# Optimization experiments

Hardware: AMD Instinct MI355X
Metric: run time of the kernel (lower is better)

Reference implementation:

```python
import jax, jax.numpy as jnp
import numpy as np

B, S, D, H = 2, 4096, 512, 8
DK = D // H


def setup_inputs() -> dict:
    key = jax.random.key(0)
    ks = jax.random.split(key, 8)
    q = jax.random.normal(ks[0], (B, S, D), dtype=jnp.float32)
    k = jax.random.normal(ks[1], (B, S, D), dtype=jnp.float32)
    v = jax.random.normal(ks[2], (B, S, D), dtype=jnp.float32)
    mask = jax.random.randint(ks[3], (B, S, S), 0, 2, dtype=jnp.int32)
    scale = 1.0 / np.sqrt(D)
    w_q = jax.random.normal(ks[4], (D, D), dtype=jnp.float32) * scale
    w_k = jax.random.normal(ks[5], (D, D), dtype=jnp.float32) * scale
    w_v = jax.random.normal(ks[6], (D, D), dtype=jnp.float32) * scale
    w_o = jax.random.normal(ks[7], (D, D), dtype=jnp.float32) * scale
    return {"q": q, "k": k, "v": v, "mask": mask,
            "w_q": w_q, "w_k": w_k, "w_v": w_v, "w_o": w_o}


def reference(q, k, v, mask, w_q, w_k, w_v, w_o):
    # Projections (weights stored as [in, out]; no bias, matching bias=False)
    # [B,S,D] -> [B,H,S,DK]
    def split_heads(x):
        return x.reshape(B, S, H, DK).transpose(0, 2, 1, 3)

    qh = split_heads(q @ w_q)
    kh = split_heads(k @ w_k)
    vh = split_heads(v @ w_v)

    inv_sqrt_dk = jnp.float32(1.0 / np.sqrt(DK))
    # Explicit O(S^2) score matrix, as in the original module
    scores = jnp.einsum('bhqd,bhkd->bhqk', qh, kh) * inv_sqrt_dk
    scores = jnp.where(mask[:, None, :, :] == 0, jnp.float32(-1e9), scores)
    attn = jax.nn.softmax(scores, axis=-1)
    # dropout in eval mode (p=0) -> identity
    x = jnp.einsum('bhqk,bhkd->bhqd', attn, vh)
    x = x.transpose(0, 2, 1, 3).reshape(B, S, D)
    return x @ w_o
```

## Files before the change

kernel.cpp:

```cpp
#include <hip/hip_runtime.h>
#include <hip/hip_bf16.h>

#define Bn 2
#define Sn 4096
#define Dn 512
#define Hn 8
#define DKn 64

typedef __attribute__((ext_vector_type(8))) short bf16x8;
typedef __attribute__((ext_vector_type(4))) float f32x4;
typedef __attribute__((ext_vector_type(4))) _Float16 f16x4;
typedef __attribute__((ext_vector_type(8))) _Float16 f16x8;
typedef __attribute__((ext_vector_type(2))) _Float16 f16x2;
typedef __attribute__((ext_vector_type(8))) unsigned short us8;
typedef __attribute__((ext_vector_type(4))) unsigned short us4;

__device__ __forceinline__ unsigned short f2bf(float f) {
  unsigned u = __builtin_bit_cast(unsigned, f);
  u += 0x7fffu + ((u >> 16) & 1u);
  return (unsigned short)(u >> 16);
}

__device__ __forceinline__ unsigned cvtpk_bf16(float lo, float hi) {
  unsigned r;
  asm("v_cvt_pk_bf16_f32 %0, %1, %2" : "=v"(r) : "v"(lo), "v"(hi));
  return r;
}

__device__ __forceinline__ unsigned spread4(unsigned x) {
  x = (x | (x << 12)) & 0x000F000Fu;
  x = (x | (x << 6)) & 0x03030303u;
  x = (x | (x << 3)) & 0x11111111u;
  return x;
}

__global__ __launch_bounds__(256) void prep_k(
    const int* __restrict__ mask, unsigned int* __restrict__ pm,
    const float* __restrict__ wq, const float* __restrict__ wk,
    const float* __restrict__ wv, const float* __restrict__ wo,
    unsigned short* __restrict__ wt) {
  const int t = threadIdx.x;
  if (blockIdx.x < 256) {
    __shared__ unsigned short ls[64][68];
    int bid = blockIdx.x;
    int z = bid >> 6, x = bid & 7, y = (bid >> 3) & 7;
    const float* W = z == 0 ? wq : z == 1 ? wk : z == 2 ? wv : wo;
    const float wsc = (z == 0) ? 0.18033688011112042f : 1.0f;
    int k0 = x * 64, n0 = y * 64;
    for (int j = 0; j < 4; ++j) {
      int i = t + j * 256;
      int r = i >> 4, c4 = (i & 15) << 2;
      float4 f = *(const float4*)&W[(size_t)(k0 + r) * 512 + n0 + c4];
      ls[c4 + 0][r] = f2bf(f.x * wsc);
      ls[c4 + 1][r] = f2bf(f.y * wsc);
      ls[c4 + 2][r] = f2bf(f.z * wsc);
      ls[c4 + 3][r] = f2bf(f.w * wsc);
    }
    __syncthreads();
    unsigned short* out = wt + (size_t)z * 512 * 512;
    for (int j = 0; j < 4; ++j) {
      int i = t + j * 256;
      int r = i >> 4, c4 = (i & 15) << 2;
      us4 v = {ls[r][c4], ls[r][c4 + 1], ls[r][c4 + 2], ls[r][c4 + 3]};
      *(us4*)&out[(size_t)(n0 + r) * 512 + k0 + c4] = v;
    }
  } else {
    size_t gt = (size_t)(blockIdx.x - 256) * 256 + t;
    for (int it = 0; it < 8; ++it, gt += 1048576) {
      size_t e0 = gt * 4;
      int4 mv = *(const int4*)&mask[e0];
      unsigned long long bl0 = __ballot(mv.x != 0);
      unsigned long long bl1 = __ballot(mv.y != 0);
      unsigned long long bl2 = __ballot(mv.z != 0);
      unsigned long long bl3 = __ballot(mv.w != 0);
      if ((t & 63) < 8) {
        int wd = t & 7;
        unsigned word = spread4((unsigned)(bl0 >> (wd * 8)) & 0xFFu) |
                        (spread4((unsigned)(bl1 >> (wd * 8)) & 0xFFu) << 1) |
                        (spread4((unsigned)(bl2 >> (wd * 8)) & 0xFFu) << 2) |
                        (spread4((unsigned)(bl3 >> (wd * 8)) & 0xFFu) << 3);
        size_t eb = e0 & ~(size_t)255;
        int qq = (int)((eb >> 12) & 4095);
        int bb = (int)(eb >> 24);
        int kvw = (int)((eb >> 5) & 127) + wd;
        pm[((size_t)bb * 128 + kvw) * 4096 + qq] = word;
      }
    }
  }
}

template <int MT, bool HEADS>
__global__ __launch_bounds__(256, 2) void gemm_k(
    const float* __restrict__ aq, const float* __restrict__ ak,
    const float* __restrict__ av, const unsigned short* __restrict__ abf,
    const unsigned short* __restrict__ wt, unsigned short* __restrict__ oh,
    unsigned short* __restrict__ vtg, float* __restrict__ olin) {
  __shared__ unsigned short smem[MT * 8192 + 16384];
  const int z = blockIdx.z;
  const float* A32 = HEADS ? (z == 0 ? aq : z == 1 ? ak : av) : nullptr;
  const unsigned short* Wt = wt + (size_t)z * 512 * 512;
  const int m0 = blockIdx.x * (MT * 64), n0 = blockIdx.y * 128;
  const int t = threadIdx.x, w = t >> 6, l = t & 63;
  const int quad = l >> 4, c = l & 15;

  f32x4 acc[MT][8] = {};
  us8 apre[MT * 2], bpre[4];

  auto ldA = [&](int j, int kk) -> us8 {
    int i = t + j * 256, r = i >> 3, u = i & 7;
    if constexpr (HEADS) {
      const float* s = &A32[(size_t)(m0 + r) * 512 + kk + (u << 3)];
      float4 f0 = *(const float4*)s;
      float4 f1 = *(const float4*)(s + 4);
      uint4 p;
      p.x = cvtpk_bf16(f0.x, f0.y);
      p.y = cvtpk_bf16(f0.z, f0.w);
      p.z = cvtpk_bf16(f1.x, f1.y);
      p.w = cvtpk_bf16(f1.z, f1.w);
      return __builtin_bit_cast(us8, p);
    } else {
      return *(const us8*)&abf[(size_t)(m0 + r) * 512 + kk + (u << 3)];
    }
  };

#pragma unroll
  for (int j = 0; j < MT * 2; ++j) apre[j] = ldA(j, 0);
#pragma unroll
  for (int j = 0; j < 4; ++j) {
    int i = t + j * 256, r = i >> 3, u = i & 7;
    bpre[j] = *(const us8*)&Wt[(size_t)(n0 + r) * 512 + (u << 3)];
  }
#pragma unroll
  for (int j = 0; j < MT * 2; ++j) {
    int i = t + j * 256, r = i >> 3, u = i & 7;
    *(us8*)&smem[r * 64 + ((u ^ (r & 7)) << 3)] = apre[j];
  }
#pragma unroll
  for (int j = 0; j < 4; ++j) {
    int i = t + j * 256, r = i >> 3, u = i & 7;
    *(us8*)&smem[MT * 8192 + r * 64 + ((u ^ (r & 7)) << 3)] = bpre[j];
  }

  for (int k0 = 0; k0 < 512; k0 += 64) {
    const int cur = (k0 >> 6) & 1;
    const unsigned short* AsC = &smem[cur * (MT * 4096)];
    const unsigned short* BsC = &smem[MT * 8192 + cur * 8192];
    __syncthreads();
    const bool nxt = k0 + 64 < 512;
    if (nxt) {
#pragma unroll
      for (int j = 0; j < MT * 2; ++j) apre[j] = ldA(j, k0 + 64);
#pragma unroll
      for (int j = 0; j < 4; ++j) {
        int i = t + j * 256, r = i >> 3, u = i & 7;
        bpre[j] = *(const us8*)&Wt[(size_t)(n0 + r) * 512 + k0 + 64 + (u << 3)];
      }
    }

#pragma unroll
    for (int kc = 0; kc < 2; ++kc) {
      bf16x8 aA[MT], bB[8];
      int u = kc * 4 + quad;
#pragma unroll
      for (int mt = 0; mt < MT; ++mt) {
        int row = w * (MT * 16) + mt * 16 + c;
        aA[mt] = *(const bf16x8*)&AsC[row * 64 + ((u ^ (c & 7)) << 3)];
      }
#pragma unroll
      for (int nt = 0; nt < 8; ++nt) {
        int row = nt * 16 + c;
        bB[nt] = *(const bf16x8*)&BsC[row * 64 + ((u ^ (c & 7)) << 3)];
      }
      __builtin_amdgcn_s_setprio(1);
#pragma unroll
      for (int mt = 0; mt < MT; ++mt)
#pragma unroll
        for (int nt = 0; nt < 8; ++nt)
          acc[mt][nt] = __builtin_amdgcn_mfma_f32_16x16x32_bf16(
              aA[mt], bB[nt], acc[mt][nt], 0, 0, 0);
      __builtin_amdgcn_s_setprio(0);
    }

    if (nxt) {
      unsigned short* AsN = &smem[(cur ^ 1) * (MT * 4096)];
      unsigned short* BsN = &smem[MT * 8192 + (cur ^ 1) * 8192];
#pragma unroll
      for (int j = 0; j < MT * 2; ++j) {
        int i = t + j * 256, r = i >> 3, u = i & 7;
        *(us8*)&AsN[r * 64 + ((u ^ (r & 7)) << 3)] = apre[j];
      }
#pragma unroll
      for (int j = 0; j < 4; ++j) {
        int i = t + j * 256, r = i >> 3, u = i & 7;
        *(us8*)&BsN[r * 64 + ((u ^ (r & 7)) << 3)] = bpre[j];
      }
    }
  }

  if constexpr (HEADS) {
    if (z == 2) {
      __syncthreads();
#pragma unroll
      for (int mt = 0; mt < MT; ++mt) {
        int mb = w * (MT * 16) + mt * 16 + (quad << 2);
        int ml = (mb & 64) | (((mb >> 5) & 1) << 5) | (((mb >> 2) & 3) << 3) |
                 (((mb >> 4) & 1) << 2);
#pragma unroll
        for (int nt = 0; nt < 8; ++nt) {
          int nl = nt * 16 + c;
          us4 pk;
#pragma unroll
          for (int r = 0; r < 4; ++r)
            pk[r] = __builtin_bit_cast(unsigned short, (_Float16)acc[mt][nt][r]);
          *(us4*)&smem[nl * 152 + ml] = pk;
        }
      }
      __syncthreads();
      const int bb = m0 >> 12, sb = m0 & 4095;
#pragma unroll
      for (int j = 0; j < MT * 4; ++j) {
        int i = t + j * 256;
        int nl = i >> 4, mc = (i & 15) << 3;
        us8 vv = *(const us8*)&smem[nl * 152 + mc];
        int n = n0 + nl, hh = n >> 6, dk = n & 63;
        *(us8*)&vtg[((size_t)(bb * Hn + hh) * DKn + dk) * Sn + sb + mc] = vv;
      }
    } else {
#pragma unroll
      for (int mt = 0; mt < MT; ++mt)
#pragma unroll
        for (int nt = 0; nt < 8; ++nt) {
          int m = m0 + w * (MT * 16) + mt * 16 + (quad << 2);
          int n = n0 + nt * 16 + c;
          int b = m >> 12, s = m & 4095, hh = n >> 6, dk = n & 63;
          unsigned short* dst = &oh[(size_t)z * (Bn * Hn * Sn * DKn) +
                                    ((size_t)(b * Hn + hh) * Sn + s) * DKn + dk];
          unsigned pk0 = cvtpk_bf16(acc[mt][nt][0], acc[mt][nt][1]);
          unsigned pk1 = cvtpk_bf16(acc[mt][nt][2], acc[mt][nt][3]);
          dst[0] = (unsigned short)pk0;
          dst[DKn] = (unsigned short)(pk0 >> 16);
          dst[2 * DKn] = (unsigned short)pk1;
          dst[3 * DKn] = (unsigned short)(pk1 >> 16);
        }
    }
  } else {
#pragma unroll
    for (int mt = 0; mt < MT; ++mt)
#pragma unroll
      for (int nt = 0; nt < 8; ++nt)
#pragma unroll
        for (int r = 0; r < 4; ++r) {
          int m = m0 + w * (MT * 16) + mt * 16 + (quad << 2) + r;
          int n = n0 + nt * 16 + c;
          olin[(size_t)m * 512 + n] = acc[mt][nt][r];
        }
  }
}

__global__ __launch_bounds__(512, 4) void flash_k(
    const unsigned short* __restrict__ Qh, const unsigned short* __restrict__ Kh,
    const unsigned short* __restrict__ VtG, const unsigned int* __restrict__ pmt,
    unsigned short* __restrict__ attn) {
  __shared__ unsigned short Ks[2][2][64 * 64];
  __shared__ unsigned short Vts[2][2][64 * 64];
  __shared__ unsigned int Mw[2][2][256];
  __shared__ unsigned long long MskT[16];

  const int bid = blockIdx.x;
  const int h = bid & 7;
  const int b = (bid >> 3) & 1;
  const int q0 = (bid >> 4) * 128;
  const int t = threadIdx.x;
  const int g = t >> 8, tg = t & 255;
  const int w = (t >> 6) & 3, l = t & 63;
  const int quad = l >> 4, c = l & 15;
  const size_t hb = (size_t)(b * Hn + h) * Sn * DKn;
  const unsigned short* Qg = Qh + hb;

  if (t < 16) {
    unsigned lo = ((t & 1) ? 0xFFFFu : 0u) | ((t & 2) ? 0xFFFF0000u : 0u);
    unsigned hi = ((t & 4) ? 0xFFFFu : 0u) | ((t & 8) ? 0xFFFF0000u : 0u);
    MskT[t] = ((unsigned long long)hi << 32) | lo;
  }

  bf16x8 bQ[2][2];
#pragma unroll
  for (int qf = 0; qf < 2; ++qf) {
    int qrow = q0 + w * 32 + qf * 16 + c;
#pragma unroll
    for (int kc = 0; kc < 2; ++kc)
      bQ[qf][kc] = *(const bf16x8*)&Qg[(size_t)qrow * 64 + kc * 32 + quad * 8];
  }

  f32x4 oacc[2][4] = {};
  f32x4 oaccl[2] = {};
  f16x8 vone8;
#pragma unroll
  for (int i = 0; i < 8; ++i) vone8[i] = (_Float16)1.0f;

  const int sr = tg >> 3, su = tg & 7;
  const int off0 = sr * 64 + ((su ^ (sr & 7)) << 3);
  const int off1 = (sr + 32) * 64 + ((su ^ (sr & 7)) << 3);

  const unsigned short* kp0 = Kh + hb + ((size_t)(g * 64 + sr)) * 64 + (su << 3);
  const unsigned short* kp1 = kp0 + 32 * 64;
  const unsigned short* vp0 = VtG + hb + (size_t)sr * Sn + g * 64 + (su << 3);
  const unsigned short* vp1 = VtG + hb + (size_t)(sr + 32) * Sn + g * 64 + (su << 3);
  const unsigned int* mp =
      pmt + ((size_t)b * 128 + g * 2 + (tg >> 7)) * 4096 + q0 + (tg & 127);

  us8 kpre[2], vpre[2];
  unsigned mpre;
  kpre[0] = *(const us8*)kp0;
  kpre[1] = *(const us8*)kp1;
  vpre[0] = *(const us8*)vp0;
  vpre[1] = *(const us8*)vp1;
  mpre = *mp;
  *(us8*)&Ks[g][0][off0] = kpre[0];
  *(us8*)&Ks[g][0][off1] = kpre[1];
  *(us8*)&Vts[g][0][off0] = vpre[0];
  *(us8*)&Vts[g][0][off1] = vpre[1];
  Mw[g][0][tg] = mpre;

  for (int it = 0; it < 32; ++it) {
    const int cur = it & 1;
    __syncthreads();
    const bool nxt = it + 1 < 32;
    if (nxt) {
      kp0 += 8192; kp1 += 8192; vp0 += 128; vp1 += 128; mp += 16384;
      kpre[0] = *(const us8*)kp0;
      kpre[1] = *(const us8*)kp1;
      vpre[0] = *(const us8*)vp0;
      vpre[1] = *(const us8*)vp1;
      mpre = *mp;
    }

    f32x4 sacc[2][4] = {};
#pragma unroll
    for (int kc = 0; kc < 2; ++kc) {
      int u = kc * 4 + quad;
#pragma unroll
      for (int kvt = 0; kvt < 4; ++kvt) {
        int row = kvt * 16 + c;
        bf16x8 aK = *(const bf16x8*)&Ks[g][cur][row * 64 + ((u ^ (c & 7)) << 3)];
#pragma unroll
        for (int qf = 0; qf < 2; ++qf)
          sacc[qf][kvt] = __builtin_amdgcn_mfma_f32_16x16x32_bf16(
              aK, bQ[qf][kc], sacc[qf][kvt], 0, 0, 0);
      }
    }

    f16x8 ph[2][2];
#pragma unroll
    for (int qf = 0; qf < 2; ++qf) {
      int qloc = w * 32 + qf * 16 + c;
      unsigned mv0 = Mw[g][cur][qloc] >> (quad << 2);
      unsigned mv1 = Mw[g][cur][128 + qloc] >> (quad << 2);
#pragma unroll
      for (int half = 0; half < 2; ++half) {
        unsigned wd = half ? mv1 : mv0;
        uint4 ww;
#pragma unroll
        for (int kvh = 0; kvh < 2; ++kvh) {
          const f32x4 s4 = sacc[qf][half * 2 + kvh];
          unsigned long long mk = MskT[(wd >> (kvh << 4)) & 15u];
          unsigned a = __builtin_bit_cast(
              unsigned, __builtin_amdgcn_cvt_pkrtz(
                            __builtin_amdgcn_exp2f(s4[0]),
                            __builtin_amdgcn_exp2f(s4[1])));
          unsigned bpk = __builtin_bit_cast(
              unsigned, __builtin_amdgcn_cvt_pkrtz(
                            __builtin_amdgcn_exp2f(s4[2]),
                            __builtin_amdgcn_exp2f(s4[3])));
          (&ww.x)[kvh * 2] = a & (unsigned)mk;
          (&ww.x)[kvh * 2 + 1] = bpk & (unsigned)(mk >> 32);
        }
        ph[qf][half] = __builtin_bit_cast(f16x8, ww);
      }
    }

#pragma unroll
    for (int half = 0; half < 2; ++half) {
      int u2 = half * 4 + quad;
#pragma unroll
      for (int dkt = 0; dkt < 4; ++dkt) {
        int dk = dkt * 16 + c;
        f16x8 bV = __builtin_bit_cast(
            f16x8, *(const us8*)&Vts[g][cur][dk * 64 + ((u2 ^ (c & 7)) << 3)]);
#pragma unroll
        for (int qf = 0; qf < 2; ++qf)
          oacc[qf][dkt] = __builtin_amdgcn_mfma_f32_16x16x32_f16(
              ph[qf][half], bV, oacc[qf][dkt], 0, 0, 0);
      }
#pragma unroll
      for (int qf = 0; qf < 2; ++qf)
        oaccl[qf] = __builtin_amdgcn_mfma_f32_16x16x32_f16(
            ph[qf][half], vone8, oaccl[qf], 0, 0, 0);
    }

    if (nxt) {
      const int nb = cur ^ 1;
      *(us8*)&Ks[g][nb][off0] = kpre[0];
      *(us8*)&Ks[g][nb][off1] = kpre[1];
      *(us8*)&Vts[g][nb][off0] = vpre[0];
      *(us8*)&Vts[g][nb][off1] = vpre[1];
      Mw[g][nb][tg] = mpre;
    }
  }

  __syncthreads();
  float* fsum = (float*)&Ks[0][0][0];
  float* flsum = (float*)&Vts[0][0][0];
  if (g == 1) {
#pragma unroll
    for (int qf = 0; qf < 2; ++qf) {
#pragma unroll
      for (int dkt = 0; dkt < 4; ++dkt)
        *(f32x4*)&fsum[(((qf * 4 + dkt) * 4 + w) * 64 + l) * 4] = oacc[qf][dkt];
      *(f32x4*)&flsum[((qf * 4 + w) * 64 + l) * 4] = oaccl[qf];
    }
  }
  __syncthreads();
  if (g == 0) {
#pragma unroll
    for (int qf = 0; qf < 2; ++qf) {
      f32x4 l1 = *(const f32x4*)&flsum[((qf * 4 + w) * 64 + l) * 4];
#pragma unroll
      for (int r = 0; r < 4; ++r) oaccl[qf][r] += l1[r];
#pragma unroll
      for (int dkt = 0; dkt < 4; ++dkt) {
        f32x4 o1 = *(const f32x4*)&fsum[(((qf * 4 + dkt) * 4 + w) * 64 + l) * 4];
#pragma unroll
        for (int r = 0; r < 4; ++r) oacc[qf][dkt][r] += o1[r];
      }
    }
#pragma unroll
    for (int qf = 0; qf < 2; ++qf)
#pragma unroll
      for (int r = 0; r < 4; ++r) {
        float invr = 1.0f / oaccl[qf][r];
        unsigned short* dst =
            &attn[((size_t)(b * Sn + q0 + w * 32 + qf * 16 + (quad << 2) + r)) * Dn +
                  h * 64 + c];
#pragma unroll
        for (int dkt = 0; dkt < 4; ++dkt)
          dst[dkt * 16] = f2bf(oacc[qf][dkt][r] * invr);
      }
  }
}

extern "C" void kernel_launch(void* const* d_in, const int* in_sizes, int n_in,
                              void* d_out, int out_size, void* d_ws,
                              size_t ws_size, hipStream_t stream) {
  const float* q = (const float*)d_in[0];
  const float* k = (const float*)d_in[1];
  const float* v = (const float*)d_in[2];
  const int* mask = (const int*)d_in[3];
  const float* wq = (const float*)d_in[4];
  const float* wk = (const float*)d_in[5];
  const float* wv = (const float*)d_in[6];
  const float* wo = (const float*)d_in[7];
  float* out = (float*)d_out;

  char* ws = (char*)d_ws;
  const size_t headN = (size_t)Bn * Hn * Sn * DKn;
  const size_t tensB = headN * 2;
  unsigned short* attn = (unsigned short*)ws;
  size_t off = 3 * tensB;
  unsigned short* qkv = (unsigned short*)(ws + off);
  off += 3 * tensB;
  unsigned short* wt = (unsigned short*)(ws + off);
  off += 4ull * 512 * 512 * 2;
  unsigned int* pm = (unsigned int*)(ws + off);

  prep_k<<<4352, 256, 0, stream>>>(mask, pm, wq, wk, wv, wo, wt);
  gemm_k<2, true><<<dim3(64, 4, 3), 256, 0, stream>>>(
      q, k, v, nullptr, wt, qkv, qkv + 2 * headN, nullptr);
  flash_k<<<dim3(512), 512, 0, stream>>>(qkv, qkv + headN,
                                         qkv + 2 * headN, pm, attn);
  gemm_k<1, false><<<dim3(128, 4, 1), 256, 0, stream>>>(
      nullptr, nullptr, nullptr, attn, wt + 3ull * 512 * 512, nullptr, nullptr,
      out);
}
```

Measured before the change: 348.5 us.

## Split flash attention key tiles across four wave groups per block

```diff
diff --git a/kernel.cpp b/kernel.cpp
--- a/kernel.cpp
+++ b/kernel.cpp
@@ -257,13 +257,11 @@
   }
 }
 
-__global__ __launch_bounds__(512, 4) void flash_k(
+__global__ __launch_bounds__(1024, 8) void flash_k(
     const unsigned short* __restrict__ Qh, const unsigned short* __restrict__ Kh,
     const unsigned short* __restrict__ VtG, const unsigned int* __restrict__ pmt,
     unsigned short* __restrict__ attn) {
-  __shared__ unsigned short Ks[2][2][64 * 64];
-  __shared__ unsigned short Vts[2][2][64 * 64];
-  __shared__ unsigned int Mw[2][2][256];
+  __shared__ unsigned short SM[34816];
   __shared__ unsigned long long MskT[16];
 
   const int bid = blockIdx.x;
@@ -276,6 +274,7 @@
   const int quad = l >> 4, c = l & 15;
   const size_t hb = (size_t)(b * Hn + h) * Sn * DKn;
   const unsigned short* Qg = Qh + hb;
+  unsigned int* MwU = (unsigned int*)(SM + 32768);
 
   if (t < 16) {
     unsigned lo = ((t & 1) ? 0xFFFFu : 0u) | ((t & 2) ? 0xFFFF0000u : 0u);
@@ -299,50 +298,46 @@
   for (int i = 0; i < 8; ++i) vone8[i] = (_Float16)1.0f;
 
   const int sr = tg >> 3, su = tg & 7;
-  const int off0 = sr * 64 + ((su ^ (sr & 7)) << 3);
-  const int off1 = (sr + 32) * 64 + ((su ^ (sr & 7)) << 3);
-
-  const unsigned short* kp0 = Kh + hb + ((size_t)(g * 64 + sr)) * 64 + (su << 3);
-  const unsigned short* kp1 = kp0 + 32 * 64;
-  const unsigned short* vp0 = VtG + hb + (size_t)sr * Sn + g * 64 + (su << 3);
-  const unsigned short* vp1 = VtG + hb + (size_t)(sr + 32) * Sn + g * 64 + (su << 3);
+  const int dk = tg >> 2, pu = tg & 3;
+  const int offK = sr * 64 + ((su ^ (sr & 7)) << 3);
+  const int offV = dk * 32 + ((pu ^ ((dk >> 1) & 3)) << 3);
+
+  const unsigned short* kp = Kh + hb + (size_t)(g * 32 + sr) * 64 + (su << 3);
+  const unsigned short* vp = VtG + hb + (size_t)dk * Sn + g * 32 + (pu << 3);
   const unsigned int* mp =
-      pmt + ((size_t)b * 128 + g * 2 + (tg >> 7)) * 4096 + q0 + (tg & 127);
-
-  us8 kpre[2], vpre[2];
+      pmt + ((size_t)b * 128 + g) * 4096 + q0 + (tg & 127);
+
+  us8 kpre, vpre;
   unsigned mpre;
-  kpre[0] = *(const us8*)kp0;
-  kpre[1] = *(const us8*)kp1;
-  vpre[0] = *(const us8*)vp0;
-  vpre[1] = *(const us8*)vp1;
-  mpre = *mp;
-  *(us8*)&Ks[g][0][off0] = kpre[0];
-  *(us8*)&Ks[g][0][off1] = kpre[1];
-  *(us8*)&Vts[g][0][off0] = vpre[0];
-  *(us8*)&Vts[g][0][off1] = vpre[1];
-  Mw[g][0][tg] = mpre;
+  kpre = *(const us8*)kp;
+  vpre = *(const us8*)vp;
+  mpre = (tg < 128) ? *mp : 0u;
+  *(us8*)&SM[(g << 1) * 2048 + offK] = kpre;
+  *(us8*)&SM[16384 + (g << 1) * 2048 + offV] = vpre;
+  if (tg < 128) MwU[(g << 1) * 128 + tg] = mpre;
 
   for (int it = 0; it < 32; ++it) {
     const int cur = it & 1;
     __syncthreads();
     const bool nxt = it + 1 < 32;
     if (nxt) {
-      kp0 += 8192; kp1 += 8192; vp0 += 128; vp1 += 128; mp += 16384;
-      kpre[0] = *(const us8*)kp0;
-      kpre[1] = *(const us8*)kp1;
-      vpre[0] = *(const us8*)vp0;
-      vpre[1] = *(const us8*)vp1;
-      mpre = *mp;
-    }
-
-    f32x4 sacc[2][4] = {};
+      kp += 8192; vp += 128; mp += 16384;
+      kpre = *(const us8*)kp;
+      vpre = *(const us8*)vp;
+      if (tg < 128) mpre = *mp;
+    }
+
+    const unsigned short* Ksb = &SM[((g << 1) | cur) * 2048];
+    const unsigned short* Vtb = &SM[16384 + ((g << 1) | cur) * 2048];
+
+    f32x4 sacc[2][2] = {};
 #pragma unroll
     for (int kc = 0; kc < 2; ++kc) {
       int u = kc * 4 + quad;
 #pragma unroll
-      for (int kvt = 0; kvt < 4; ++kvt) {
+      for (int kvt = 0; kvt < 2; ++kvt) {
         int row = kvt * 16 + c;
-        bf16x8 aK = *(const bf16x8*)&Ks[g][cur][row * 64 + ((u ^ (c & 7)) << 3)];
+        bf16x8 aK = *(const bf16x8*)&Ksb[row * 64 + ((u ^ (c & 7)) << 3)];
 #pragma unroll
         for (int qf = 0; qf < 2; ++qf)
           sacc[qf][kvt] = __builtin_amdgcn_mfma_f32_16x16x32_bf16(
@@ -350,90 +345,85 @@
       }
     }
 
-    f16x8 ph[2][2];
+    f16x8 ph[2];
 #pragma unroll
     for (int qf = 0; qf < 2; ++qf) {
       int qloc = w * 32 + qf * 16 + c;
-      unsigned mv0 = Mw[g][cur][qloc] >> (quad << 2);
-      unsigned mv1 = Mw[g][cur][128 + qloc] >> (quad << 2);
-#pragma unroll
-      for (int half = 0; half < 2; ++half) {
-        unsigned wd = half ? mv1 : mv0;
-        uint4 ww;
-#pragma unroll
-        for (int kvh = 0; kvh < 2; ++kvh) {
-          const f32x4 s4 = sacc[qf][half * 2 + kvh];
-          unsigned long long mk = MskT[(wd >> (kvh << 4)) & 15u];
-          unsigned a = __builtin_bit_cast(
-              unsigned, __builtin_amdgcn_cvt_pkrtz(
-                            __builtin_amdgcn_exp2f(s4[0]),
-                            __builtin_amdgcn_exp2f(s4[1])));
-          unsigned bpk = __builtin_bit_cast(
-              unsigned, __builtin_amdgcn_cvt_pkrtz(
-                            __builtin_amdgcn_exp2f(s4[2]),
-                            __builtin_amdgcn_exp2f(s4[3])));
-          (&ww.x)[kvh * 2] = a & (unsigned)mk;
-          (&ww.x)[kvh * 2 + 1] = bpk & (unsigned)(mk >> 32);
-        }
-        ph[qf][half] = __builtin_bit_cast(f16x8, ww);
-      }
-    }
-
-#pragma unroll
-    for (int half = 0; half < 2; ++half) {
-      int u2 = half * 4 + quad;
-#pragma unroll
-      for (int dkt = 0; dkt < 4; ++dkt) {
-        int dk = dkt * 16 + c;
-        f16x8 bV = __builtin_bit_cast(
-            f16x8, *(const us8*)&Vts[g][cur][dk * 64 + ((u2 ^ (c & 7)) << 3)]);
-#pragma unroll
-        for (int qf = 0; qf < 2; ++qf)
-          oacc[qf][dkt] = __builtin_amdgcn_mfma_f32_16x16x32_f16(
-              ph[qf][half], bV, oacc[qf][dkt], 0, 0, 0);
-      }
+      unsigned wd = MwU[((g << 1) | cur) * 128 + qloc] >> (quad << 2);
+      uint4 ww;
+#pragma unroll
+      for (int kvh = 0; kvh < 2; ++kvh) {
+        const f32x4 s4 = sacc[qf][kvh];
+        unsigned long long mk = MskT[(wd >> (kvh << 4)) & 15u];
+        unsigned a = __builtin_bit_cast(
+            unsigned, __builtin_amdgcn_cvt_pkrtz(
+                          __builtin_amdgcn_exp2f(s4[0]),
+                          __builtin_amdgcn_exp2f(s4[1])));
+        unsigned bpk = __builtin_bit_cast(
+            unsigned, __builtin_amdgcn_cvt_pkrtz(
+                          __builtin_amdgcn_exp2f(s4[2]),
+                          __builtin_amdgcn_exp2f(s4[3])));
+        (&ww.x)[kvh * 2] = a & (unsigned)mk;
+        (&ww.x)[kvh * 2 + 1] = bpk & (unsigned)(mk >> 32);
+      }
+      ph[qf] = __builtin_bit_cast(f16x8, ww);
+    }
+
+#pragma unroll
+    for (int dkt = 0; dkt < 4; ++dkt) {
+      int dk2 = dkt * 16 + c;
+      f16x8 bV = __builtin_bit_cast(
+          f16x8,
+          *(const us8*)&Vtb[dk2 * 32 + ((quad ^ ((c >> 1) & 3)) << 3)]);
 #pragma unroll
       for (int qf = 0; qf < 2; ++qf)
-        oaccl[qf] = __builtin_amdgcn_mfma_f32_16x16x32_f16(
-            ph[qf][half], vone8, oaccl[qf], 0, 0, 0);
-    }
+        oacc[qf][dkt] = __builtin_amdgcn_mfma_f32_16x16x32_f16(
+            ph[qf], bV, oacc[qf][dkt], 0, 0, 0);
+    }
+#pragma unroll
+    for (int qf = 0; qf < 2; ++qf)
+      oaccl[qf] = __builtin_amdgcn_mfma_f32_16x16x32_f16(
+          ph[qf], vone8, oaccl[qf], 0, 0, 0);
 
     if (nxt) {
       const int nb = cur ^ 1;
-      *(us8*)&Ks[g][nb][off0] = kpre[0];
-      *(us8*)&Ks[g][nb][off1] = kpre[1];
-      *(us8*)&Vts[g][nb][off0] = vpre[0];
-      *(us8*)&Vts[g][nb][off1] = vpre[1];
-      Mw[g][nb][tg] = mpre;
+      *(us8*)&SM[((g << 1) | nb) * 2048 + offK] = kpre;
+      *(us8*)&SM[16384 + ((g << 1) | nb) * 2048 + offV] = vpre;
+      if (tg < 128) MwU[((g << 1) | nb) * 128 + tg] = mpre;
     }
   }
 
   __syncthreads();
-  float* fsum = (float*)&Ks[0][0][0];
-  float* flsum = (float*)&Vts[0][0][0];
-  if (g == 1) {
-#pragma unroll
-    for (int qf = 0; qf < 2; ++qf) {
+  float* fs = (float*)SM;
+  float* fl = (float*)(SM + 24576);
+#pragma unroll
+  for (int qf = 0; qf < 2; ++qf) {
+    if (g > 0) {
+      int slot = g - 1;
 #pragma unroll
       for (int dkt = 0; dkt < 4; ++dkt)
-        *(f32x4*)&fsum[(((qf * 4 + dkt) * 4 + w) * 64 + l) * 4] = oacc[qf][dkt];
-      *(f32x4*)&flsum[((qf * 4 + w) * 64 + l) * 4] = oaccl[qf];
-    }
-  }
-  __syncthreads();
+        *(f32x4*)&fs[(((slot * 4 + dkt) * 4 + w) * 64 + l) * 4] = oacc[qf][dkt];
+      *(f32x4*)&fl[(((slot * 4 + w)) * 64 + l) * 4] = oaccl[qf];
+    }
+    __syncthreads();
+    if (g == 0) {
+#pragma unroll
+      for (int slot = 0; slot < 3; ++slot) {
+        f32x4 l1 = *(const f32x4*)&fl[(((slot * 4 + w)) * 64 + l) * 4];
+#pragma unroll
+        for (int r = 0; r < 4; ++r) oaccl[qf][r] += l1[r];
+#pragma unroll
+        for (int dkt = 0; dkt < 4; ++dkt) {
+          f32x4 o1 =
+              *(const f32x4*)&fs[(((slot * 4 + dkt) * 4 + w) * 64 + l) * 4];
+#pragma unroll
+          for (int r = 0; r < 4; ++r) oacc[qf][dkt][r] += o1[r];
+        }
+      }
+    }
+    __syncthreads();
+  }
   if (g == 0) {
-#pragma unroll
-    for (int qf = 0; qf < 2; ++qf) {
-      f32x4 l1 = *(const f32x4*)&flsum[((qf * 4 + w) * 64 + l) * 4];
-#pragma unroll
-      for (int r = 0; r < 4; ++r) oaccl[qf][r] += l1[r];
-#pragma unroll
-      for (int dkt = 0; dkt < 4; ++dkt) {
-        f32x4 o1 = *(const f32x4*)&fsum[(((qf * 4 + dkt) * 4 + w) * 64 + l) * 4];
-#pragma unroll
-        for (int r = 0; r < 4; ++r) oacc[qf][dkt][r] += o1[r];
-      }
-    }
 #pragma unroll
     for (int qf = 0; qf < 2; ++qf)
 #pragma unroll
@@ -476,8 +466,8 @@
   prep_k<<<4352, 256, 0, stream>>>(mask, pm, wq, wk, wv, wo, wt);
   gemm_k<2, true><<<dim3(64, 4, 3), 256, 0, stream>>>(
       q, k, v, nullptr, wt, qkv, qkv + 2 * headN, nullptr);
-  flash_k<<<dim3(512), 512, 0, stream>>>(qkv, qkv + headN,
-                                         qkv + 2 * headN, pm, attn);
+  flash_k<<<dim3(512), 1024, 0, stream>>>(qkv, qkv + headN,
+                                          qkv + 2 * headN, pm, attn);
   gemm_k<1, false><<<dim3(128, 4, 1), 256, 0, stream>>>(
       nullptr, nullptr, nullptr, attn, wt + 3ull * 512 * 512, nullptr, nullptr,
       out);
```

New measurement: 1.173 ms. 237% more time.
